# Optimization experiments

Measured on AMD Instinct MI355X. Metric: run time of the kernel, lower is better.

Reference implementation:

```python
import jax, jax.numpy as jnp
import numpy as np

N_NODES = 100000
N_RELS = 1000
N_EDGES = 400000
DIM = 256  # even: split into real/imag halves


def setup_inputs() -> dict:
    key = jax.random.key(0)
    k1, k2, k3, k4, k5 = jax.random.split(key, 5)
    node_emb = jax.random.normal(k1, (N_NODES, DIM), dtype=jnp.float32)
    rel_emb = jax.random.normal(k2, (N_RELS, DIM), dtype=jnp.float32)
    src = jax.random.randint(k3, (N_EDGES,), 0, N_NODES, dtype=jnp.int64 if jax.config.jax_enable_x64 else jnp.int32).astype(jnp.int32)
    dst = jax.random.randint(k4, (N_EDGES,), 0, N_NODES).astype(jnp.int32)
    rel_id = jax.random.randint(k5, (N_EDGES,), 0, N_RELS).astype(jnp.int32)
    return {"node_emb": node_emb, "rel_emb": rel_emb, "src": src, "dst": dst, "rel_id": rel_id}


def reference(node_emb, rel_emb, src, dst, rel_id):
    h = node_emb[src]      # [E, D] gathered head embeddings
    t = node_emb[dst]      # [E, D] gathered tail embeddings
    r = rel_emb[rel_id]    # [E, D] gathered relation embeddings
    half = h.shape[-1] // 2
    rh, ih = h[:, :half], h[:, half:]
    rt, it = t[:, :half], t[:, half:]
    rr, ir = r[:, :half], r[:, half:]
    # ComplEx: Re(<h, r, conj(t)>)
    score = rh * rt * rr + ih * it * rr + rh * it * ir - ih * rt * ir
    return jnp.sum(score, axis=-1)  # [E]
```

## Files before the change

kernel.cpp:

```cpp
#include <hip/hip_runtime.h>

#define DIM 256
#define HALF 128
#define N_EDGES_CONST 400000

__global__ __launch_bounds__(256) void complex_score_kernel(
    const float* __restrict__ node_emb,
    const float* __restrict__ rel_emb,
    const int* __restrict__ src,
    const int* __restrict__ dst,
    const int* __restrict__ rel_id,
    float* __restrict__ out,
    int n_edges)
{
    const int tid  = blockIdx.x * blockDim.x + threadIdx.x;
    const int edge = tid >> 5;
    const int lane = tid & 31;
    if (edge >= n_edges) return;

    const int s = src[edge];
    const int d = dst[edge];
    const int r = rel_id[edge];

    const float4* __restrict__ hp = (const float4*)(node_emb + (size_t)s * DIM);
    const float4* __restrict__ tp = (const float4*)(node_emb + (size_t)d * DIM);
    const float4* __restrict__ rp = (const float4*)(rel_emb  + (size_t)r * DIM);

    float4 rh = hp[lane];
    float4 ih = hp[lane + 32];
    float4 rt = tp[lane];
    float4 it = tp[lane + 32];
    float4 rr = rp[lane];
    float4 ir = rp[lane + 32];

    float acc;
    {
        float a0 = rr.x * (rh.x * rt.x + ih.x * it.x) + ir.x * (rh.x * it.x - ih.x * rt.x);
        float a1 = rr.y * (rh.y * rt.y + ih.y * it.y) + ir.y * (rh.y * it.y - ih.y * rt.y);
        float a2 = rr.z * (rh.z * rt.z + ih.z * it.z) + ir.z * (rh.z * it.z - ih.z * rt.z);
        float a3 = rr.w * (rh.w * rt.w + ih.w * it.w) + ir.w * (rh.w * it.w - ih.w * rt.w);
        acc = (a0 + a1) + (a2 + a3);
    }

    #pragma unroll
    for (int off = 16; off > 0; off >>= 1)
        acc += __shfl_xor(acc, off, 32);

    if (lane == 0)
        out[edge] = acc;
}

extern "C" void kernel_launch(void* const* d_in, const int* in_sizes, int n_in,
                              void* d_out, int out_size, void* d_ws, size_t ws_size,
                              hipStream_t stream) {
    const float* node_emb = (const float*)d_in[0];
    const float* rel_emb  = (const float*)d_in[1];
    const int*   src      = (const int*)d_in[2];
    const int*   dst      = (const int*)d_in[3];
    const int*   rel_id   = (const int*)d_in[4];
    float* out = (float*)d_out;

    const int n_edges = in_sizes[2];
    const int threads_per_block = 256;
    const long long total_threads = (long long)n_edges * 32;
    const int blocks = (int)((total_threads + threads_per_block - 1) / threads_per_block);

    complex_score_kernel<<<blocks, threads_per_block, 0, stream>>>(
        node_emb, rel_emb, src, dst, rel_id, out, n_edges);
}
```

Measured before the change: 246.6 us.

## Convert embedding tables to fp16 in workspace before gathering scores

Adds a pre-pass that converts node and relation embeddings to fp16 in the workspace, then runs a gather kernel that reads half-size rows and uses lane shuffles to pair real and imaginary halves. The aim is to cut the memory traffic of the random row gathers. In exchange, every call pays a full conversion pass over the node table, and accuracy drops to fp16 inputs. It falls back to the fp32 kernel when the workspace is too small.

```diff
diff --git a/kernel.cpp b/kernel.cpp
--- a/kernel.cpp
+++ b/kernel.cpp
@@ -1,10 +1,88 @@
 #include <hip/hip_runtime.h>
+#include <hip/hip_fp16.h>
+#include <string.h>
 
 #define DIM 256
-#define HALF 128
-#define N_EDGES_CONST 400000
 
-__global__ __launch_bounds__(256) void complex_score_kernel(
+__global__ __launch_bounds__(256) void f32_to_f16_kernel(
+    const float* __restrict__ in, int4* __restrict__ out, int n8)
+{
+    int i = blockIdx.x * blockDim.x + threadIdx.x;
+    if (i >= n8) return;
+    const float4* p = (const float4*)in + 2 * (size_t)i;
+    float4 a = p[0];
+    float4 b = p[1];
+    __half2 h0 = __float22half2_rn(make_float2(a.x, a.y));
+    __half2 h1 = __float22half2_rn(make_float2(a.z, a.w));
+    __half2 h2 = __float22half2_rn(make_float2(b.x, b.y));
+    __half2 h3 = __float22half2_rn(make_float2(b.z, b.w));
+    int4 o;
+    memcpy(&o.x, &h0, 4);
+    memcpy(&o.y, &h1, 4);
+    memcpy(&o.z, &h2, 4);
+    memcpy(&o.w, &h3, 4);
+    out[i] = o;
+}
+
+__global__ __launch_bounds__(256) void complex_score_f16_kernel(
+    const __half* __restrict__ node,
+    const __half* __restrict__ rel,
+    const int* __restrict__ src,
+    const int* __restrict__ dst,
+    const int* __restrict__ rid,
+    float* __restrict__ out,
+    int n_edges)
+{
+    const int tid  = blockIdx.x * blockDim.x + threadIdx.x;
+    const int edge = tid >> 5;
+    const int lane = tid & 31;
+    if (edge >= n_edges) return;
+
+    const int s = src[edge];
+    const int d = dst[edge];
+    const int r = rid[edge];
+
+    const int4* hp = (const int4*)(node + (size_t)s * DIM);
+    const int4* tp = (const int4*)(node + (size_t)d * DIM);
+    const int4* rp = (const int4*)(rel  + (size_t)r * DIM);
+
+    int4 hv = hp[lane];
+    int4 tv = tp[lane];
+    int4 rv = rp[lane];
+
+    int4 hq, tq;
+    hq.x = __shfl_xor(hv.x, 16); hq.y = __shfl_xor(hv.y, 16);
+    hq.z = __shfl_xor(hv.z, 16); hq.w = __shfl_xor(hv.w, 16);
+    tq.x = __shfl_xor(tv.x, 16); tq.y = __shfl_xor(tv.y, 16);
+    tq.z = __shfl_xor(tv.z, 16); tq.w = __shfl_xor(tv.w, 16);
+
+    const bool hi = (lane & 16) != 0;
+    float acc = 0.0f;
+
+    #define UP(v, f2) { __half2 _h; memcpy(&_h, &(v), 4); f2 = __half22float2(_h); }
+    #define TERM(c) { \
+        float2 oh, ph, ot, pt, rr; \
+        UP(hv.c, oh); UP(hq.c, ph); \
+        UP(tv.c, ot); UP(tq.c, pt); \
+        UP(rv.c, rr); \
+        float tx = hi ? (ph.x * ot.x - oh.x * pt.x) : (oh.x * ot.x + ph.x * pt.x); \
+        float ty = hi ? (ph.y * ot.y - oh.y * pt.y) : (oh.y * ot.y + ph.y * pt.y); \
+        acc = fmaf(rr.x, tx, acc); \
+        acc = fmaf(rr.y, ty, acc); }
+
+    TERM(x) TERM(y) TERM(z) TERM(w)
+    #undef TERM
+    #undef UP
+
+    #pragma unroll
+    for (int off = 16; off > 0; off >>= 1)
+        acc += __shfl_xor(acc, off);
+
+    if (lane == 0)
+        out[edge] = acc;
+}
+
+__global__ __launch_bounds__(256) void complex_score_f32_kernel(
     const float* __restrict__ node_emb,
     const float* __restrict__ rel_emb,
     const int* __restrict__ src,
@@ -22,9 +100,9 @@
     const int d = dst[edge];
     const int r = rel_id[edge];
 
-    const float4* __restrict__ hp = (const float4*)(node_emb + (size_t)s * DIM);
-    const float4* __restrict__ tp = (const float4*)(node_emb + (size_t)d * DIM);
-    const float4* __restrict__ rp = (const float4*)(rel_emb  + (size_t)r * DIM);
+    const float4* hp = (const float4*)(node_emb + (size_t)s * DIM);
+    const float4* tp = (const float4*)(node_emb + (size_t)d * DIM);
+    const float4* rp = (const float4*)(rel_emb  + (size_t)r * DIM);
 
     float4 rh = hp[lane];
     float4 ih = hp[lane + 32];
@@ -33,14 +111,11 @@
     float4 rr = rp[lane];
     float4 ir = rp[lane + 32];
 
-    float acc;
-    {
-        float a0 = rr.x * (rh.x * rt.x + ih.x * it.x) + ir.x * (rh.x * it.x - ih.x * rt.x);
-        float a1 = rr.y * (rh.y * rt.y + ih.y * it.y) + ir.y * (rh.y * it.y - ih.y * rt.y);
-        float a2 = rr.z * (rh.z * rt.z + ih.z * it.z) + ir.z * (rh.z * it.z - ih.z * rt.z);
-        float a3 = rr.w * (rh.w * rt.w + ih.w * it.w) + ir.w * (rh.w * it.w - ih.w * rt.w);
-        acc = (a0 + a1) + (a2 + a3);
-    }
+    float a0 = rr.x * (rh.x * rt.x + ih.x * it.x) + ir.x * (rh.x * it.x - ih.x * rt.x);
+    float a1 = rr.y * (rh.y * rt.y + ih.y * it.y) + ir.y * (rh.y * it.y - ih.y * rt.y);
+    float a2 = rr.z * (rh.z * rt.z + ih.z * it.z) + ir.z * (rh.z * it.z - ih.z * rt.z);
+    float a3 = rr.w * (rh.w * rt.w + ih.w * it.w) + ir.w * (rh.w * it.w - ih.w * rt.w);
+    float acc = (a0 + a1) + (a2 + a3);
 
     #pragma unroll
     for (int off = 16; off > 0; off >>= 1)
@@ -61,10 +136,31 @@
     float* out = (float*)d_out;
 
     const int n_edges = in_sizes[2];
-    const int threads_per_block = 256;
+    const int n_nodes = in_sizes[0] / DIM;
+    const int n_rels  = in_sizes[1] / DIM;
+
+    const size_t f16_bytes = ((size_t)n_nodes + (size_t)n_rels) * DIM * 2;
+
+    const int tpb = 256;
     const long long total_threads = (long long)n_edges * 32;
-    const int blocks = (int)((total_threads + threads_per_block - 1) / threads_per_block);
+    const int score_blocks = (int)((total_threads + tpb - 1) / tpb);
 
-    complex_score_kernel<<<blocks, threads_per_block, 0, stream>>>(
-        node_emb, rel_emb, src, dst, rel_id, out, n_edges);
+    if (ws_size >= f16_bytes) {
+        __half* node_f16 = (__half*)d_ws;
+        __half* rel_f16  = node_f16 + (size_t)n_nodes * DIM;
+
+        const int n8_node = n_nodes * DIM / 8;
+        const int n8_rel  = n_rels  * DIM / 8;
+
+        f32_to_f16_kernel<<<(n8_node + tpb - 1) / tpb, tpb, 0, stream>>>(
+            node_emb, (int4*)node_f16, n8_node);
+        f32_to_f16_kernel<<<(n8_rel + tpb - 1) / tpb, tpb, 0, stream>>>(
+            rel_emb, (int4*)rel_f16, n8_rel);
+
+        complex_score_f16_kernel<<<score_blocks, tpb, 0, stream>>>(
+            node_f16, rel_f16, src, dst, rel_id, out, n_edges);
+    } else {
+        complex_score_f32_kernel<<<score_blocks, tpb, 0, stream>>>(
+            node_emb, rel_emb, src, dst, rel_id, out, n_edges);
+    }
 }
```

Result: faster. 226.0 us (-8.4%).
